# Performance work log

Hardware: AMD Instinct MI355X
Metric: run time of the kernel (lower is better)

The kernel has to match this reference:

```python
import jax, jax.numpy as jnp
import numpy as np

B = 65536
IN = 64
H = 128
OUT = 2


def setup_inputs() -> dict:
    key = jax.random.key(0)
    ks = jax.random.split(key, 16)
    s_in = 1.0 / np.sqrt(IN)
    s_h = 1.0 / np.sqrt(H)
    d = {}
    d["x"] = jax.random.normal(ks[0], (B, IN), dtype=jnp.float32)
    # initial state (module resets to zeros per day)
    d["h0"] = jnp.zeros((H,), dtype=jnp.float32)
    d["c0"] = jnp.zeros((B, H), dtype=jnp.float32)
    # input->hidden linears (with bias), torch Linear layout [out, in]
    for i, name in enumerate(["f", "i", "o", "c"]):
        d[f"Wx{name}"] = jax.random.uniform(ks[1 + i], (H, IN), jnp.float32, -s_in, s_in)
        d[f"bx{name}"] = jax.random.uniform(ks[5 + i], (H,), jnp.float32, -s_in, s_in)
        d[f"Wh{name}"] = jax.random.uniform(ks[9 + i], (H, H), jnp.float32, -s_h, s_h)
    d["Wy"] = jax.random.uniform(ks[13], (OUT, H), jnp.float32, -s_h, s_h)
    d["by"] = jax.random.uniform(ks[14], (OUT,), jnp.float32, -s_h, s_h)
    return d


def reference(x, h0, c0, Wxf, bxf, Wxi, bxi, Wxo, bxo, Wxc, bxc, Whf, Whi, Who, Whc, Wy, by):
    # hidden recurrent contributions (h0 is a length-H vector, broadcast over batch)
    hi = h0 @ Whi.T  # [H]
    hf = h0 @ Whf.T
    ho = h0 @ Who.T
    hc = h0 @ Whc.T
    i = jax.nn.sigmoid(x @ Wxi.T + bxi + hi)  # [B, H]
    f = jax.nn.sigmoid(x @ Wxf.T + bxf + hf)
    o = jax.nn.sigmoid(x @ Wxo.T + bxo + ho)
    c_til = jnp.tanh(x @ Wxc.T + bxc + hc)
    c = f * c0 + i * c_til
    h = o * jnp.tanh(c)
    y_hat = h @ Wy.T + by  # [B, OUT]
    return y_hat
```

## Files before the change

### kernel.cpp

```cpp
#include <hip/hip_runtime.h>


#define B_SIZE 65536

typedef __bf16 bf16x8 __attribute__((ext_vector_type(8)));
typedef __bf16 bf16x4 __attribute__((ext_vector_type(4)));
typedef float f32x4 __attribute__((ext_vector_type(4)));

#define LOG2E 1.442695040888963f
#define TWO_LOG2E 2.885390081777927f

__device__ __forceinline__ float ftanh(float x) {
    float e = __builtin_amdgcn_exp2f(TWO_LOG2E * x);
    return 1.0f - 2.0f * __builtin_amdgcn_rcpf(e + 1.0f);
}

__global__ void prep_kernel(const float* __restrict__ h0,
                            const float* __restrict__ Whf, const float* __restrict__ Whi,
                            const float* __restrict__ Who, const float* __restrict__ Whc,
                            const float* __restrict__ bxf, const float* __restrict__ bxi,
                            const float* __restrict__ bxo, const float* __restrict__ bxc,
                            const float* __restrict__ Wxf, const float* __restrict__ Wxi,
                            const float* __restrict__ Wxo, const float* __restrict__ Wxc,
                            float* __restrict__ bias512, __bf16* __restrict__ frags) {
    if (blockIdx.x < 8) {
        int j = blockIdx.x * 64 + threadIdx.x;
        int g = j >> 7, r = j & 127;
        const float* Wh = (g == 0) ? Whf : (g == 1) ? Whi : (g == 2) ? Who : Whc;
        const float* bx = (g == 0) ? bxf : (g == 1) ? bxi : (g == 2) ? bxo : bxc;
        const float sg = (g == 3) ? TWO_LOG2E : -LOG2E;
        float s = bx[r];
        const float4* row = (const float4*)(Wh + r * 128);
        const float4* h4  = (const float4*)h0;
#pragma unroll 8
        for (int k = 0; k < 32; ++k) {
            float4 a = row[k], b = h4[k];
            s += a.x * b.x + a.y * b.y + a.z * b.z + a.w * b.w;
        }
        bias512[j] = s * sg;
    } else {
        int t = (blockIdx.x - 8) * 64 + threadIdx.x;
        int w    = t >> 10;
        int g    = (t >> 8) & 3;
        int cb   = (t >> 7) & 1;
        int kb   = (t >> 6) & 1;
        int lane = t & 63;
        const float* Wx = (g == 0) ? Wxf : (g == 1) ? Wxi : (g == 2) ? Wxo : Wxc;
        const float sg = (g == 3) ? TWO_LOG2E : -LOG2E;
        const int n = w * 32 + cb * 16 + (lane & 15);
        const float* p = Wx + n * 64 + kb * 32 + (lane >> 4) * 8;
        float4 lo = *(const float4*)p;
        float4 hi = *(const float4*)(p + 4);
        bf16x8 v;
        v[0] = (__bf16)(lo.x * sg); v[1] = (__bf16)(lo.y * sg);
        v[2] = (__bf16)(lo.z * sg); v[3] = (__bf16)(lo.w * sg);
        v[4] = (__bf16)(hi.x * sg); v[5] = (__bf16)(hi.y * sg);
        v[6] = (__bf16)(hi.z * sg); v[7] = (__bf16)(hi.w * sg);
        *(bf16x8*)(frags + (size_t)t * 8) = v;
    }
}

__launch_bounds__(256, 2)
__global__ void lstm_kernel(const float* __restrict__ x, const float* __restrict__ c0,
                            const __bf16* __restrict__ frags,
                            const float* __restrict__ Wy, const float* __restrict__ by,
                            const float* __restrict__ bias512, float* __restrict__ out) {
    __shared__ __bf16 xs[2][1024];
    __shared__ float cs[2][16 * 132];
    __shared__ float yred[4][128][8];

    const int tid  = threadIdx.x;
    const int lane = tid & 63;
    const int w    = tid >> 6;
    const int q    = lane >> 4;
    const int n15  = lane & 15;

    bf16x8 bw[4][2][2];
    float biasv[4][2];
#pragma unroll
    for (int g = 0; g < 4; ++g)
#pragma unroll
        for (int cb = 0; cb < 2; ++cb) {
            biasv[g][cb] = bias512[g * 128 + w * 32 + cb * 16 + n15];
#pragma unroll
            for (int kb = 0; kb < 2; ++kb)
                bw[g][cb][kb] = *(const bf16x8*)(frags +
                    (size_t)(((w * 16 + g * 4 + cb * 2 + kb) * 64 + lane)) * 8);
        }
    float wyv[2][2];
#pragma unroll
    for (int o = 0; o < 2; ++o)
#pragma unroll
        for (int cb = 0; cb < 2; ++cb)
            wyv[o][cb] = Wy[o * 128 + w * 32 + cb * 16 + n15];
    const float by0 = by[0], by1 = by[1];

    constexpr int ITERS = (B_SIZE / 16) / 512;
    const int tile0 = blockIdx.x * ITERS;

    const int xrow = tid >> 4;
    const int k4   = (tid & 15) * 4;
    const int sidx = (k4 >> 5) * 512 + ((k4 & 31) >> 3) * 128 + xrow * 8 + (k4 & 7);

    const int ccol = (tid & 15) * 8;
    const int cidx = xrow * 132 + ccol;

    float4 xr[2], cpa[2], cpb[2];

    xr[0]  = *(const float4*)(x  + (size_t)(tile0 * 16 + xrow) * 64 + k4);
    cpa[0] = *(const float4*)(c0 + (size_t)(tile0 * 16 + xrow) * 128 + ccol);
    cpb[0] = *(const float4*)(c0 + (size_t)(tile0 * 16 + xrow) * 128 + ccol + 4);
    {
        bf16x4 v; v[0] = (__bf16)xr[0].x; v[1] = (__bf16)xr[0].y;
        v[2] = (__bf16)xr[0].z; v[3] = (__bf16)xr[0].w;
        *(bf16x4*)&xs[0][sidx] = v;
        *(float4*)&cs[0][cidx] = cpa[0];
        *(float4*)&cs[0][cidx + 4] = cpb[0];
    }
    xr[0]  = *(const float4*)(x  + (size_t)((tile0 + 1) * 16 + xrow) * 64 + k4);
    cpa[0] = *(const float4*)(c0 + (size_t)((tile0 + 1) * 16 + xrow) * 128 + ccol);
    cpb[0] = *(const float4*)(c0 + (size_t)((tile0 + 1) * 16 + xrow) * 128 + ccol + 4);
    __syncthreads();

#pragma unroll
    for (int it = 0; it < ITERS; ++it) {
        const int cur = it & 1;
        const int hs  = it & 1;
        const int fs  = hs ^ 1;

        if (it + 2 < ITERS) {
            const int tn = tile0 + it + 2;
            xr[fs]  = *(const float4*)(x  + (size_t)(tn * 16 + xrow) * 64 + k4);
            cpa[fs] = *(const float4*)(c0 + (size_t)(tn * 16 + xrow) * 128 + ccol);
            cpb[fs] = *(const float4*)(c0 + (size_t)(tn * 16 + xrow) * 128 + ccol + 4);
        }

        bf16x8 a0 = *(const bf16x8*)&xs[cur][lane * 8];
        bf16x8 a1 = *(const bf16x8*)&xs[cur][512 + lane * 8];

        float c0v[2][4];
#pragma unroll
        for (int cb = 0; cb < 2; ++cb)
#pragma unroll
            for (int r = 0; r < 4; ++r)
                c0v[cb][r] = cs[cur][(q * 4 + r) * 132 + w * 32 + cb * 16 + n15];

        f32x4 acc[4][2];
#pragma unroll
        for (int g = 0; g < 4; ++g)
#pragma unroll
            for (int cb = 0; cb < 2; ++cb) {
                float b = biasv[g][cb];
                f32x4 t = {b, b, b, b};
                acc[g][cb] = t;
            }
#pragma unroll
        for (int g = 0; g < 4; ++g)
#pragma unroll
            for (int cb = 0; cb < 2; ++cb) {
                acc[g][cb] = __builtin_amdgcn_mfma_f32_16x16x32_bf16(a0, bw[g][cb][0], acc[g][cb], 0, 0, 0);
                acc[g][cb] = __builtin_amdgcn_mfma_f32_16x16x32_bf16(a1, bw[g][cb][1], acc[g][cb], 0, 0, 0);
            }

        float p0[4] = {0.f, 0.f, 0.f, 0.f};
        float p1[4] = {0.f, 0.f, 0.f, 0.f};
#pragma unroll
        for (int cb = 0; cb < 2; ++cb)
#pragma unroll
            for (int r = 0; r < 4; ++r) {
                float fg = __builtin_amdgcn_rcpf(1.0f + __builtin_amdgcn_exp2f(acc[0][cb][r]));
                float ig = __builtin_amdgcn_rcpf(1.0f + __builtin_amdgcn_exp2f(acc[1][cb][r]));
                float og = __builtin_amdgcn_rcpf(1.0f + __builtin_amdgcn_exp2f(acc[2][cb][r]));
                float ec = __builtin_amdgcn_exp2f(acc[3][cb][r]);
                float ct = 1.0f - 2.0f * __builtin_amdgcn_rcpf(ec + 1.0f);
                float c  = fg * c0v[cb][r] + ig * ct;
                float h  = og * ftanh(c);
                p0[r] += h * wyv[0][cb];
                p1[r] += h * wyv[1][cb];
            }
#pragma unroll
        for (int m = 1; m < 4; m <<= 1) {
#pragma unroll
            for (int r = 0; r < 4; ++r) {
                p0[r] += __shfl_xor(p0[r], m, 64);
                p1[r] += __shfl_xor(p1[r], m, 64);
            }
        }
        if ((n15 & 3) == 0) {
            const int part = n15 >> 2;
#pragma unroll
            for (int r = 0; r < 4; ++r) {
                yred[w][it * 16 + q * 4 + r][part]     = p0[r];
                yred[w][it * 16 + q * 4 + r][4 + part] = p1[r];
            }
        }

        if (it + 1 < ITERS) {
            bf16x4 v; v[0] = (__bf16)xr[hs].x; v[1] = (__bf16)xr[hs].y;
            v[2] = (__bf16)xr[hs].z; v[3] = (__bf16)xr[hs].w;
            *(bf16x4*)&xs[cur ^ 1][sidx] = v;
            *(float4*)&cs[cur ^ 1][cidx] = cpa[hs];
            *(float4*)&cs[cur ^ 1][cidx + 4] = cpb[hs];
        }
        __syncthreads();
    }

    if (tid < 128) {
        float s0 = by0, s1 = by1;
#pragma unroll
        for (int w2 = 0; w2 < 4; ++w2)
#pragma unroll
            for (int p = 0; p < 4; ++p) {
                s0 += yred[w2][tid][p];
                s1 += yred[w2][tid][4 + p];
            }
        float2 s = {s0, s1};
        *(float2*)(out + (size_t)(tile0 * 16 + tid) * 2) = s;
    }
}

extern "C" void kernel_launch(void* const* d_in, const int* in_sizes, int n_in,
                              void* d_out, int out_size, void* d_ws, size_t ws_size,
                              hipStream_t stream) {
    const float* x   = (const float*)d_in[0];
    const float* h0  = (const float*)d_in[1];
    const float* c0  = (const float*)d_in[2];
    const float* Wxf = (const float*)d_in[3];
    const float* bxf = (const float*)d_in[4];
    const float* Whf = (const float*)d_in[5];
    const float* Wxi = (const float*)d_in[6];
    const float* bxi = (const float*)d_in[7];
    const float* Whi = (const float*)d_in[8];
    const float* Wxo = (const float*)d_in[9];
    const float* bxo = (const float*)d_in[10];
    const float* Who = (const float*)d_in[11];
    const float* Wxc = (const float*)d_in[12];
    const float* bxc = (const float*)d_in[13];
    const float* Whc = (const float*)d_in[14];
    const float* Wy  = (const float*)d_in[15];
    const float* by  = (const float*)d_in[16];
    float* out = (float*)d_out;
    float* bias512 = (float*)d_ws;
    __bf16* frags  = (__bf16*)((float*)d_ws + 512);

    prep_kernel<<<72, 64, 0, stream>>>(h0, Whf, Whi, Who, Whc, bxf, bxi, bxo, bxc,
                                       Wxf, Wxi, Wxo, Wxc, bias512, frags);
    lstm_kernel<<<512, 256, 0, stream>>>(x, c0, frags, Wy, by, bias512, out);
}
```

Baseline: 128.5 us.

## Load x and c0 directly into registers and reduce outputs with atomics

Drops the LDS double-buffered staging of x and c0 and the per-iteration barriers. Each lane now loads its MFMA A-fragment and its c0 values straight from global memory. The cross-wave output reduction through shared memory is replaced by a full 16-lane shuffle reduction followed by float atomicAdd into out, which the prep kernel pre-initializes with the bias by. This removes LDS traffic and synchronization, but the c0 loads become scalar and strided (non-float4), prefetching is lost, and 4 waves contend with atomics on each output element.

```diff
diff --git a/kernel.cpp b/kernel.cpp
--- a/kernel.cpp
+++ b/kernel.cpp
@@ -4,7 +4,6 @@
 #define B_SIZE 65536
 
 typedef __bf16 bf16x8 __attribute__((ext_vector_type(8)));
-typedef __bf16 bf16x4 __attribute__((ext_vector_type(4)));
 typedef float f32x4 __attribute__((ext_vector_type(4)));
 
 #define LOG2E 1.442695040888963f
@@ -22,7 +21,9 @@
                             const float* __restrict__ bxo, const float* __restrict__ bxc,
                             const float* __restrict__ Wxf, const float* __restrict__ Wxi,
                             const float* __restrict__ Wxo, const float* __restrict__ Wxc,
-                            float* __restrict__ bias512, __bf16* __restrict__ frags) {
+                            const float* __restrict__ by,
+                            float* __restrict__ bias512, __bf16* __restrict__ frags,
+                            float* __restrict__ out) {
     if (blockIdx.x < 8) {
         int j = blockIdx.x * 64 + threadIdx.x;
         int g = j >> 7, r = j & 127;
@@ -38,7 +39,7 @@
             s += a.x * b.x + a.y * b.y + a.z * b.z + a.w * b.w;
         }
         bias512[j] = s * sg;
-    } else {
+    } else if (blockIdx.x < 72) {
         int t = (blockIdx.x - 8) * 64 + threadIdx.x;
         int w    = t >> 10;
         int g    = (t >> 8) & 3;
@@ -57,18 +58,18 @@
         v[4] = (__bf16)(hi.x * sg); v[5] = (__bf16)(hi.y * sg);
         v[6] = (__bf16)(hi.z * sg); v[7] = (__bf16)(hi.w * sg);
         *(bf16x8*)(frags + (size_t)t * 8) = v;
+    } else {
+        int idx = (blockIdx.x - 72) * 64 + threadIdx.x;
+        float4 v = {by[0], by[1], by[0], by[1]};
+        *(float4*)(out + (size_t)idx * 4) = v;
     }
 }
 
 __launch_bounds__(256, 2)
 __global__ void lstm_kernel(const float* __restrict__ x, const float* __restrict__ c0,
                             const __bf16* __restrict__ frags,
-                            const float* __restrict__ Wy, const float* __restrict__ by,
+                            const float* __restrict__ Wy,
                             const float* __restrict__ bias512, float* __restrict__ out) {
-    __shared__ __bf16 xs[2][1024];
-    __shared__ float cs[2][16 * 132];
-    __shared__ float yred[4][128][8];
-
     const int tid  = threadIdx.x;
     const int lane = tid & 63;
     const int w    = tid >> 6;
@@ -93,57 +94,32 @@
 #pragma unroll
         for (int cb = 0; cb < 2; ++cb)
             wyv[o][cb] = Wy[o * 128 + w * 32 + cb * 16 + n15];
-    const float by0 = by[0], by1 = by[1];
 
     constexpr int ITERS = (B_SIZE / 16) / 512;
     const int tile0 = blockIdx.x * ITERS;
 
-    const int xrow = tid >> 4;
-    const int k4   = (tid & 15) * 4;
-    const int sidx = (k4 >> 5) * 512 + ((k4 & 31) >> 3) * 128 + xrow * 8 + (k4 & 7);
-
-    const int ccol = (tid & 15) * 8;
-    const int cidx = xrow * 132 + ccol;
-
-    float4 xr[2], cpa[2], cpb[2];
-
-    xr[0]  = *(const float4*)(x  + (size_t)(tile0 * 16 + xrow) * 64 + k4);
-    cpa[0] = *(const float4*)(c0 + (size_t)(tile0 * 16 + xrow) * 128 + ccol);
-    cpb[0] = *(const float4*)(c0 + (size_t)(tile0 * 16 + xrow) * 128 + ccol + 4);
-    {
-        bf16x4 v; v[0] = (__bf16)xr[0].x; v[1] = (__bf16)xr[0].y;
-        v[2] = (__bf16)xr[0].z; v[3] = (__bf16)xr[0].w;
-        *(bf16x4*)&xs[0][sidx] = v;
-        *(float4*)&cs[0][cidx] = cpa[0];
-        *(float4*)&cs[0][cidx + 4] = cpb[0];
-    }
-    xr[0]  = *(const float4*)(x  + (size_t)((tile0 + 1) * 16 + xrow) * 64 + k4);
-    cpa[0] = *(const float4*)(c0 + (size_t)((tile0 + 1) * 16 + xrow) * 128 + ccol);
-    cpb[0] = *(const float4*)(c0 + (size_t)((tile0 + 1) * 16 + xrow) * 128 + ccol + 4);
-    __syncthreads();
-
-#pragma unroll
+#pragma unroll 2
     for (int it = 0; it < ITERS; ++it) {
-        const int cur = it & 1;
-        const int hs  = it & 1;
-        const int fs  = hs ^ 1;
-
-        if (it + 2 < ITERS) {
-            const int tn = tile0 + it + 2;
-            xr[fs]  = *(const float4*)(x  + (size_t)(tn * 16 + xrow) * 64 + k4);
-            cpa[fs] = *(const float4*)(c0 + (size_t)(tn * 16 + xrow) * 128 + ccol);
-            cpb[fs] = *(const float4*)(c0 + (size_t)(tn * 16 + xrow) * 128 + ccol + 4);
-        }
-
-        bf16x8 a0 = *(const bf16x8*)&xs[cur][lane * 8];
-        bf16x8 a1 = *(const bf16x8*)&xs[cur][512 + lane * 8];
+        const int b0 = (tile0 + it) * 16;
+
+        const float* xp = x + (size_t)(b0 + n15) * 64 + q * 8;
+        float4 xa = *(const float4*)(xp);
+        float4 xb = *(const float4*)(xp + 4);
+        float4 xc = *(const float4*)(xp + 32);
+        float4 xd = *(const float4*)(xp + 36);
 
         float c0v[2][4];
 #pragma unroll
         for (int cb = 0; cb < 2; ++cb)
 #pragma unroll
             for (int r = 0; r < 4; ++r)
-                c0v[cb][r] = cs[cur][(q * 4 + r) * 132 + w * 32 + cb * 16 + n15];
+                c0v[cb][r] = c0[(size_t)(b0 + q * 4 + r) * 128 + w * 32 + cb * 16 + n15];
+
+        bf16x8 a0, a1;
+        a0[0] = (__bf16)xa.x; a0[1] = (__bf16)xa.y; a0[2] = (__bf16)xa.z; a0[3] = (__bf16)xa.w;
+        a0[4] = (__bf16)xb.x; a0[5] = (__bf16)xb.y; a0[6] = (__bf16)xb.z; a0[7] = (__bf16)xb.w;
+        a1[0] = (__bf16)xc.x; a1[1] = (__bf16)xc.y; a1[2] = (__bf16)xc.z; a1[3] = (__bf16)xc.w;
+        a1[4] = (__bf16)xd.x; a1[5] = (__bf16)xd.y; a1[6] = (__bf16)xd.z; a1[7] = (__bf16)xd.w;
 
         f32x4 acc[4][2];
 #pragma unroll
@@ -179,43 +155,20 @@
                 p1[r] += h * wyv[1][cb];
             }
 #pragma unroll
-        for (int m = 1; m < 4; m <<= 1) {
+        for (int m = 1; m < 16; m <<= 1) {
 #pragma unroll
             for (int r = 0; r < 4; ++r) {
                 p0[r] += __shfl_xor(p0[r], m, 64);
                 p1[r] += __shfl_xor(p1[r], m, 64);
             }
         }
-        if ((n15 & 3) == 0) {
-            const int part = n15 >> 2;
+        if (n15 == 0) {
 #pragma unroll
             for (int r = 0; r < 4; ++r) {
-                yred[w][it * 16 + q * 4 + r][part]     = p0[r];
-                yred[w][it * 16 + q * 4 + r][4 + part] = p1[r];
-            }
-        }
-
-        if (it + 1 < ITERS) {
-            bf16x4 v; v[0] = (__bf16)xr[hs].x; v[1] = (__bf16)xr[hs].y;
-            v[2] = (__bf16)xr[hs].z; v[3] = (__bf16)xr[hs].w;
-            *(bf16x4*)&xs[cur ^ 1][sidx] = v;
-            *(float4*)&cs[cur ^ 1][cidx] = cpa[hs];
-            *(float4*)&cs[cur ^ 1][cidx + 4] = cpb[hs];
-        }
-        __syncthreads();
-    }
-
-    if (tid < 128) {
-        float s0 = by0, s1 = by1;
-#pragma unroll
-        for (int w2 = 0; w2 < 4; ++w2)
-#pragma unroll
-            for (int p = 0; p < 4; ++p) {
-                s0 += yred[w2][tid][p];
-                s1 += yred[w2][tid][4 + p];
-            }
-        float2 s = {s0, s1};
-        *(float2*)(out + (size_t)(tile0 * 16 + tid) * 2) = s;
+                atomicAdd(out + (size_t)(b0 + q * 4 + r) * 2,     p0[r]);
+                atomicAdd(out + (size_t)(b0 + q * 4 + r) * 2 + 1, p1[r]);
+            }
+        }
     }
 }
 
@@ -243,7 +196,7 @@
     float* bias512 = (float*)d_ws;
     __bf16* frags  = (__bf16*)((float*)d_ws + 512);
 
-    prep_kernel<<<72, 64, 0, stream>>>(h0, Whf, Whi, Who, Whc, bxf, bxi, bxo, bxc,
-                                       Wxf, Wxi, Wxo, Wxc, bias512, frags);
-    lstm_kernel<<<512, 256, 0, stream>>>(x, c0, frags, Wy, by, bias512, out);
-}
+    prep_kernel<<<584, 64, 0, stream>>>(h0, Whf, Whi, Who, Whc, bxf, bxi, bxo, bxc,
+                                        Wxf, Wxi, Wxo, Wxc, by, bias512, frags, out);
+    lstm_kernel<<<512, 256, 0, stream>>>(x, c0, frags, Wy, bias512, out);
+}
```

Result: no change. 129.3 us (+0.6%).
